# Optimization experiments

Measured on AMD Instinct MI355X. Metric: run time of the kernel, lower is better.

Reference implementation:

```python
import jax, jax.numpy as jnp
import numpy as np

EPS = 1e-8
LAMBDA_SOFTMAX = 20.0
TEMPERATURE = 0.05


def l2norm(x, axis):
    # matches torch: x / (sqrt(sum(x^2)) + eps)
    return x / (jnp.sqrt(jnp.sum(x * x, axis=axis, keepdims=True)) + EPS)


def func_attention_fast(query, context, query_mask, context_mask):
    """query (Bq,Lq,d), context (Bc,Ls,d), query_mask (Bq,Lq,1), context_mask (Bc,1,Ls).
    Returns weightedContext (Bc,Bq,Lq,d)."""
    q = l2norm(query, -1)
    c = l2norm(context, -1)
    # context.unsqueeze(1) @ query^T -> (Bc,Bq,Ls,Lq)
    attn = jnp.einsum('csd,qld->cqsl', c, q)
    attn = jnp.where(attn > 0, attn, 0.1 * attn)  # LeakyReLU(0.1)
    attn = l2norm(attn, 3)                        # normalize over Lq axis
    attn = jnp.transpose(attn, (0, 1, 3, 2))      # (Bc,Bq,Lq,Ls)
    attn = attn + query_mask[None] + context_mask[:, None]
    attn = jax.nn.softmax(attn * LAMBDA_SOFTMAX, axis=-1)
    # focal_type='prob' -> funcH = 1.0
    re_attn = attn / jnp.sum(attn, axis=-1, keepdims=True)
    # contextT @ re_attnT then transpose -> (Bc,Bq,Lq,d)
    return jnp.einsum('csd,cqls->cqld', c, re_attn)


def cosine_sim(x1, x2):
    w12 = jnp.sum(x1 * x2, axis=-1)
    w1 = jnp.linalg.norm(x1, axis=-1)
    w2 = jnp.linalg.norm(x2, axis=-1)
    return w12 / jnp.clip(w1 * w2, 1e-8)


def xattn_score_fast(images, captions, img_mask, cap_mask):
    # i2t: attend image regions for each caption word
    wei = func_attention_fast(captions, images, cap_mask[:, :, None], img_mask[:, None, :])
    i2t_sim = cosine_sim(captions[None], wei).mean(axis=-1)   # (n_img, n_cap)
    # t2i: attend caption words for each image region
    wei = func_attention_fast(images, captions, img_mask[:, :, None], cap_mask[:, None, :])
    t2i_sim = cosine_sim(images[None], wei).mean(axis=-1)     # (n_cap, n_img)
    return t2i_sim.T + i2t_sim                                # (n_img, n_cap)


def norm_softmax_loss(x):
    i_logsm = jax.nn.log_softmax(x / TEMPERATURE, axis=1)
    j_logsm = jax.nn.log_softmax(x.T / TEMPERATURE, axis=1)
    return -jnp.mean(jnp.diag(i_logsm)) - jnp.mean(jnp.diag(j_logsm))


def rwa_loss(im, s, im_m, s_m):
    scores = xattn_score_fast(im, s, im_m, s_m)               # (B,B)
    labels = jnp.eye(im.shape[0], dtype=scores.dtype)
    logits = scores * LAMBDA_SOFTMAX
    pred = jax.nn.softmax(logits, axis=1)
    loss = pred * (jax.nn.log_softmax(logits, axis=1) - jnp.log(labels + 1e-6))
    return jnp.mean(jnp.sum(loss, axis=1))


def setup_inputs() -> dict:
    key = jax.random.key(0)
    k1, k2, k3, k4 = jax.random.split(key, 4)
    B, Lr, Lw, d = 128, 64, 32, 512
    return {
        'global_sim': jax.random.normal(k1, (B, B), dtype=jnp.float32),
        'local_im': jax.random.normal(k2, (B, Lr, d), dtype=jnp.float32),
        'local_s': jax.random.normal(k3, (B, Lw, d), dtype=jnp.float32),
        'local_im_m': jnp.zeros((B, Lr), dtype=jnp.float32),
        'local_s_l': jax.random.randint(k4, (B,), 1, Lw, dtype=jnp.int32),
        'local_s_m': jnp.zeros((B, Lw), dtype=jnp.float32),
    }


def reference(global_sim, local_im, local_s, local_im_m, local_s_l, local_s_m):
    # use_local=True, use_global=True (local_s_l is unused in the fast path)
    global_loss = norm_softmax_loss(global_sim)
    local_loss = rwa_loss(local_im, local_s, local_im_m, local_s_m)
    loss = global_loss + local_loss
    return (loss, global_loss, local_loss)
```

## Files before the change

### kernel.cpp

```cpp
#include <hip/hip_runtime.h>
#include <math.h>

#define EPSF 1e-8f
#define LAM 20.0f

typedef short short8 __attribute__((ext_vector_type(8)));
typedef float f32x4 __attribute__((ext_vector_type(4)));

__device__ __forceinline__ unsigned short f2bf(float x) {
  unsigned u = __float_as_uint(x);
  u += 0x7fffu + ((u >> 16) & 1u);
  return (unsigned short)(u >> 16);
}
__device__ __forceinline__ float bf2f(unsigned short h) {
  return __uint_as_float(((unsigned)h) << 16);
}

__global__ __launch_bounds__(256) void norm_convert(
    const float* __restrict__ im, const float* __restrict__ s,
    float* __restrict__ nim, float* __restrict__ ns,
    unsigned short* __restrict__ imn, unsigned short* __restrict__ sn,
    float* __restrict__ acc) {
  if (blockIdx.x == 0 && threadIdx.x < 4) acc[threadIdx.x] = 0.f;
  int row = blockIdx.x * 4 + (threadIdx.x >> 6);
  int lane = threadIdx.x & 63;
  const float* src;
  unsigned short* dst;
  float* ndst;
  if (row < 8192) {
    src = im + ((size_t)row << 9);
    dst = imn + ((size_t)row << 9);
    ndst = nim + row;
  } else {
    int r = row - 8192;
    src = s + ((size_t)r << 9);
    dst = sn + ((size_t)r << 9);
    ndst = ns + r;
  }
  float4 v0 = ((const float4*)src)[lane * 2];
  float4 v1 = ((const float4*)src)[lane * 2 + 1];
  float ss = 0.f;
  ss = fmaf(v0.x, v0.x, ss); ss = fmaf(v0.y, v0.y, ss);
  ss = fmaf(v0.z, v0.z, ss); ss = fmaf(v0.w, v0.w, ss);
  ss = fmaf(v1.x, v1.x, ss); ss = fmaf(v1.y, v1.y, ss);
  ss = fmaf(v1.z, v1.z, ss); ss = fmaf(v1.w, v1.w, ss);
#pragma unroll
  for (int o = 32; o; o >>= 1) ss += __shfl_xor(ss, o);
  float n = sqrtf(ss);
  if (lane == 0) *ndst = n;
  float ci = 1.0f / (n + EPSF);
  union { unsigned short us[8]; uint4 v; } p;
  p.us[0] = f2bf(v0.x * ci); p.us[1] = f2bf(v0.y * ci);
  p.us[2] = f2bf(v0.z * ci); p.us[3] = f2bf(v0.w * ci);
  p.us[4] = f2bf(v1.x * ci); p.us[5] = f2bf(v1.y * ci);
  p.us[6] = f2bf(v1.z * ci); p.us[7] = f2bf(v1.w * ci);
  ((uint4*)dst)[lane] = p.v;
}

template <int LS>
__device__ __forceinline__ void gram_body(const unsigned short* __restrict__ ctxn,
                                          unsigned short* __restrict__ Gbf,
                                          int c, char* sm) {
  constexpr int RW = (LS / 16) / 2;
  const int t = threadIdx.x;
  const int w = t >> 6, lane = t & 63, m16 = lane & 15, grp = lane >> 4;
  const int rT0 = (w & 1) * RW, cT0 = (w >> 1) * RW;
  const unsigned short* base = ctxn + ((size_t)c * LS << 9);
  f32x4 g[RW][RW];
#pragma unroll
  for (int ri = 0; ri < RW; ri++)
#pragma unroll
    for (int ci = 0; ci < RW; ci++) g[ri][ci] = {0.f, 0.f, 0.f, 0.f};

  for (int ch = 0; ch < 4; ch++) {
    __syncthreads();
    for (int idx = t; idx < LS * 16; idx += 256) {
      int row = idx >> 4, u = idx & 15;
      *(uint4*)(sm + row * 272 + u * 16) =
          ((const uint4*)(base + ((size_t)row << 9) + (ch << 7)))[u];
    }
    __syncthreads();
#pragma unroll
    for (int kk = 0; kk < 4; kk++) {
      short8 a[RW], b[RW];
#pragma unroll
      for (int ri = 0; ri < RW; ri++)
        a[ri] = *(const short8*)(sm + ((rT0 + ri) * 16 + m16) * 272 + kk * 64 + grp * 16);
#pragma unroll
      for (int ci = 0; ci < RW; ci++)
        b[ci] = *(const short8*)(sm + ((cT0 + ci) * 16 + m16) * 272 + kk * 64 + grp * 16);
#pragma unroll
      for (int ri = 0; ri < RW; ri++)
#pragma unroll
        for (int ci = 0; ci < RW; ci++)
          g[ri][ci] = __builtin_amdgcn_mfma_f32_16x16x32_bf16(a[ri], b[ci], g[ri][ci], 0, 0, 0);
    }
  }
#pragma unroll
  for (int ri = 0; ri < RW; ri++)
#pragma unroll
    for (int ci = 0; ci < RW; ci++)
#pragma unroll
      for (int r = 0; r < 4; r++) {
        int s = (rT0 + ri) * 16 + grp * 4 + r;
        int sp = (cT0 + ci) * 16 + m16;
        Gbf[(size_t)c * LS * LS + s * LS + sp] = f2bf(g[ri][ci][r]);
      }
}

__global__ __launch_bounds__(256, 2) void gram_all(
    const unsigned short* __restrict__ imn, const unsigned short* __restrict__ sn,
    unsigned short* __restrict__ Gim, unsigned short* __restrict__ Gs) {
  __shared__ __align__(16) char sm[64 * 272];
  if (blockIdx.x < 128) gram_body<64>(imn, Gim, blockIdx.x, sm);
  else gram_body<32>(sn, Gs, blockIdx.x - 128, sm);
}

__global__ __launch_bounds__(256, 3) void attn_pair(
    const unsigned short* __restrict__ imn, const unsigned short* __restrict__ sn,
    const unsigned short* __restrict__ Gim, const unsigned short* __restrict__ Gs,
    const float* __restrict__ nim, const float* __restrict__ ns,
    const float* __restrict__ im_m, const float* __restrict__ s_m,
    float* __restrict__ i2t, float* __restrict__ t2i) {
  constexpr int SROW = 144;
  constexpr int S0P = 264;
  constexpr int GOFF = 256 * SROW;
  constexpr int FOFF = GOFF + 8192;
  constexpr int POFF = 33792;
  __shared__ __align__(16) char sm[FOFF + 2056 * 4];
  float* F = (float*)(sm + FOFF);
  float* rinv_i = F;
  float* cmv_i = F + 512;
  float* cmmax_i = F + 640;
  float* rinv_t = F + 644;
  float* sevt = F + 900;
  float* wn2t = F + 1412;
  float* cmv_t = F + 1924;
  float* cmmax_t = F + 2052;
  float* sumev_i = F + 644;
  float* psum = (float*)(sm + GOFF);

  const int bq = blockIdx.x;
  const int bc = blockIdx.y;
  const int t = threadIdx.x;
  const int w = t >> 6, lane = t & 63, m16 = lane & 15, grp = lane >> 4;
  auto soff = [](int n) { return n * S0P; };

  const unsigned short* aBase = imn + ((size_t)bc << 16);
  const unsigned short* bBase = sn + ((size_t)bq << 16);

  if (t < 128) cmv_i[t] = im_m[bc * 128 + t];
  else cmv_t[t - 128] = s_m[bq * 128 + (t - 128)];
  const int c3 = w >> 1, hf = w & 1;
  short8 g_a[2][2];
  {
    const unsigned short* gB = Gim + ((size_t)bc * 2 + c3) * 4096;
#pragma unroll
    for (int mi = 0; mi < 2; mi++) {
      int sp = (hf * 2 + mi) * 16 + m16;
#pragma unroll
      for (int ks = 0; ks < 2; ks++)
        g_a[mi][ks] = *(const short8*)(gB + sp * 64 + ks * 32 + grp * 8);
    }
  }

  f32x4 regs[16];
#pragma unroll
  for (int i = 0; i < 16; i++) regs[i] = {0.f, 0.f, 0.f, 0.f};

  const int sT0 = (w & 1) * 4, nT0 = (w >> 1) * 4;
  for (int ch = 0; ch < 8; ch++) {
    __syncthreads();
#pragma unroll
    for (int i = 0; i < 8; i++) {
      int idx = t + i * 256;
      int row = idx >> 3, u = idx & 7;
      const unsigned short* src =
          (row < 128) ? (aBase + ((size_t)row << 9)) : (bBase + ((size_t)(row - 128) << 9));
      *(uint4*)(sm + row * SROW + u * 16) = *(const uint4*)(src + ch * 64 + u * 8);
    }
    __syncthreads();
#pragma unroll
    for (int kk = 0; kk < 2; kk++) {
      short8 av[4], bv[4];
#pragma unroll
      for (int si = 0; si < 4; si++)
        av[si] = *(const short8*)(sm + ((sT0 + si) * 16 + m16) * SROW + kk * 64 + grp * 16);
#pragma unroll
      for (int ni = 0; ni < 4; ni++)
        bv[ni] = *(const short8*)(sm + (128 + (nT0 + ni) * 16 + m16) * SROW + kk * 64 + grp * 16);
#pragma unroll
      for (int si = 0; si < 4; si++)
#pragma unroll
        for (int ni = 0; ni < 4; ni++)
          regs[si * 4 + ni] = __builtin_amdgcn_mfma_f32_16x16x32_bf16(
              av[si], bv[ni], regs[si * 4 + ni], 0, 0, 0);
    }
  }
  __syncthreads();
#pragma unroll
  for (int si = 0; si < 4; si++)
#pragma unroll
    for (int ni = 0; ni < 4; ni++) {
      int n = (nT0 + ni) * 16 + m16;
      int m0 = (sT0 + si) * 16 + grp * 4;
      f32x4 a = regs[si * 4 + ni];
      ushort4 p;
      p.x = f2bf(a[0]); p.y = f2bf(a[1]);
      p.z = f2bf(a[2]); p.w = f2bf(a[3]);
      *(ushort4*)(sm + soff(n) + m0 * 2) = p;
    }
  __syncthreads();

  if (t < 128) {
    if (t < 2) {
      float mx = cmv_i[t * 64];
      for (int s = 1; s < 64; s++) mx = fmaxf(mx, cmv_i[t * 64 + s]);
      cmmax_i[t] = mx;
    } else if (t < 6) {
      int ci = t - 2;
      float mx = cmv_t[ci * 32];
      for (int s = 1; s < 32; s++) mx = fmaxf(mx, cmv_t[ci * 32 + s]);
      cmmax_t[ci] = mx;
    }
    int qi = t >> 5, mg = (t & 31) * 4;
    float s0 = 0.f, s1 = 0.f, s2 = 0.f, s3 = 0.f;
    for (int l = 0; l < 32; l++) {
      uint2 pk = *(const uint2*)(sm + soff(qi * 32 + l) + mg * 2);
      float v0 = __uint_as_float(pk.x << 16);
      float v1 = __uint_as_float(pk.x & 0xffff0000u);
      float v2 = __uint_as_float(pk.y << 16);
      float v3 = __uint_as_float(pk.y & 0xffff0000u);
      v0 = v0 > 0.f ? v0 : 0.1f * v0;
      v1 = v1 > 0.f ? v1 : 0.1f * v1;
      v2 = v2 > 0.f ? v2 : 0.1f * v2;
      v3 = v3 > 0.f ? v3 : 0.1f * v3;
      s0 = fmaf(v0, v0, s0); s1 = fmaf(v1, v1, s1);
      s2 = fmaf(v2, v2, s2); s3 = fmaf(v3, v3, s3);
    }
    rinv_i[qi * 128 + mg + 0] = 1.0f / (sqrtf(s0) + EPSF);
    rinv_i[qi * 128 + mg + 1] = 1.0f / (sqrtf(s1) + EPSF);
    rinv_i[qi * 128 + mg + 2] = 1.0f / (sqrtf(s2) + EPSF);
    rinv_i[qi * 128 + mg + 3] = 1.0f / (sqrtf(s3) + EPSF);
  } else {
    int n = t - 128;
#pragma unroll
    for (int qi = 0; qi < 2; qi++) {
      float ss = 0.f;
#pragma unroll 4
      for (int j = 0; j < 16; j++) {
        uint2 pk = *(const uint2*)(sm + soff(n) + qi * 128 + j * 8);
        float v0 = __uint_as_float(pk.x << 16);
        float v1 = __uint_as_float(pk.x & 0xffff0000u);
        float v2 = __uint_as_float(pk.y << 16);
        float v3 = __uint_as_float(pk.y & 0xffff0000u);
        v0 = v0 > 0.f ? v0 : 0.1f * v0;
        v1 = v1 > 0.f ? v1 : 0.1f * v1;
        v2 = v2 > 0.f ? v2 : 0.1f * v2;
        v3 = v3 > 0.f ? v3 : 0.1f * v3;
        ss = fmaf(v0, v0, ss); ss = fmaf(v1, v1, ss);
        ss = fmaf(v2, v2, ss); ss = fmaf(v3, v3, ss);
      }
      rinv_t[qi * 128 + n] = 1.0f / (sqrtf(ss) + EPSF);
    }
  }
  __syncthreads();

  {
    const int mp = t & 127;
    const int h = t >> 7;
    const int qi = mp >> 6;
    char* ET = sm + GOFF;
    float* P = (float*)(sm + POFF);
    const unsigned short* gB2 = Gs + ((size_t)bq << 12);
    for (int ci = 0; ci < 4; ci++) {
      short8 ga0 = *(const short8*)(gB2 + ci * 1024 + m16 * 32 + grp * 8);
      short8 ga1 = *(const short8*)(gB2 + ci * 1024 + (16 + m16) * 32 + grp * 8);
      const float mxc = LAM * (1.0f + cmmax_t[ci]);
      const float* rv = rinv_t + qi * 128 + ci * 32 + h * 16;
      const float* cv = cmv_t + ci * 32 + h * 16;
      float sev = 0.f;
      unsigned pk[8];
#pragma unroll
      for (int u = 0; u < 8; u++) {
        int s0 = ci * 32 + h * 16 + u * 2;
        float v0 = bf2f(*(const unsigned short*)(sm + soff(s0) + mp * 2));
        float v1 = bf2f(*(const unsigned short*)(sm + soff(s0 + 1) + mp * 2));
        float l0 = v0 > 0.f ? v0 : 0.1f * v0;
        float l1 = v1 > 0.f ? v1 : 0.1f * v1;
        float e0 = __expf(LAM * fmaf(l0, rv[u * 2], cv[u * 2]) - mxc);
        float e1 = __expf(LAM * fmaf(l1, rv[u * 2 + 1], cv[u * 2 + 1]) - mxc);
        sev = fmaf(e0, v0, sev);
        sev = fmaf(e1, v1, sev);
        pk[u] = (unsigned)f2bf(e0) | ((unsigned)f2bf(e1) << 16);
      }
      P[t] = sev;
      uint4 w0; w0.x = pk[0]; w0.y = pk[1]; w0.z = pk[2]; w0.w = pk[3];
      uint4 w1; w1.x = pk[4]; w1.y = pk[5]; w1.z = pk[6]; w1.w = pk[7];
      *(uint4*)(ET + mp * 64 + h * 32) = w0;
      *(uint4*)(ET + mp * 64 + h * 32 + 16) = w1;
      __syncthreads();
      if (t < 128) sevt[ci * 128 + t] = P[t] + P[t + 128];
      short8 bfrag[2];
#pragma unroll
      for (int nt = 0; nt < 2; nt++)
        bfrag[nt] = *(const short8*)(ET + ((w * 2 + nt) * 16 + m16) * 64 + grp * 16);
      f32x4 u00 = __builtin_amdgcn_mfma_f32_16x16x32_bf16(ga0, bfrag[0], (f32x4){0.f, 0.f, 0.f, 0.f}, 0, 0, 0);
      f32x4 u01 = __builtin_amdgcn_mfma_f32_16x16x32_bf16(ga0, bfrag[1], (f32x4){0.f, 0.f, 0.f, 0.f}, 0, 0, 0);
      f32x4 u10 = __builtin_amdgcn_mfma_f32_16x16x32_bf16(ga1, bfrag[0], (f32x4){0.f, 0.f, 0.f, 0.f}, 0, 0, 0);
      f32x4 u11 = __builtin_amdgcn_mfma_f32_16x16x32_bf16(ga1, bfrag[1], (f32x4){0.f, 0.f, 0.f, 0.f}, 0, 0, 0);
#pragma unroll
      for (int nt = 0; nt < 2; nt++) {
        const char* erow = ET + ((w * 2 + nt) * 16 + m16) * 64;
        float part = 0.f;
#pragma unroll
        for (int mt = 0; mt < 2; mt++) {
          uint2 ee = *(const uint2*)(erow + (mt * 16 + grp * 4) * 2);
          f32x4 uu = (mt == 0) ? (nt == 0 ? u00 : u01) : (nt == 0 ? u10 : u11);
          part += __uint_as_float(ee.x << 16) * uu[0];
          part += __uint_as_float(ee.x & 0xffff0000u) * uu[1];
          part += __uint_as_float(ee.y << 16) * uu[2];
          part += __uint_as_float(ee.y & 0xffff0000u) * uu[3];
        }
        part += __shfl_xor(part, 16);
        part += __shfl_xor(part, 32);
        if (lane < 16) wn2t[ci * 128 + (w * 2 + nt) * 16 + m16] = part;
      }
      __syncthreads();
    }
  }

  {
    const int p = t >> 5, l0 = t & 31;
    const int cc = p >> 1, qi = p & 1;
    float sum = 0.f;
#pragma unroll
    for (int li = 0; li < 2; li++) {
      int n = qi * 64 + l0 + li * 32;
      float nq = nim[bc * 128 + n];
      float sev = sevt[cc * 128 + n];
      float wn2 = wn2t[cc * 128 + n];
      float denom = fmaxf(nq * sqrtf(fmaxf(wn2, 0.f)), 1e-30f);
      sum += (nq + EPSF) * sev / denom;
    }
#pragma unroll
    for (int o = 1; o < 32; o <<= 1) sum += __shfl_xor(sum, o);
    if (l0 == 0) t2i[(bq * 4 + cc) * 128 + bc * 2 + qi] = sum * (1.0f / 64.f);
  }
  __syncthreads();

  {
    const int n = t & 127;
    const int qi = n >> 5;
    const int ci = t >> 7;
    char* rowp = sm + soff(n) + ci * 128;
    const float* rv = rinv_i + qi * 128 + ci * 64;
    const float* cv = cmv_i + ci * 64;
    const float mxc = LAM * (1.0f + cmmax_i[ci]);
    float sev = 0.f;
#pragma unroll
    for (int u = 0; u < 16; u++) {
      uint2 pk = *(const uint2*)(rowp + u * 8);
      float v0 = __uint_as_float(pk.x << 16);
      float v1 = __uint_as_float(pk.x & 0xffff0000u);
      float v2 = __uint_as_float(pk.y << 16);
      float v3 = __uint_as_float(pk.y & 0xffff0000u);
      int s = u * 4;
      float l0 = v0 > 0.f ? v0 : 0.1f * v0;
      float l1 = v1 > 0.f ? v1 : 0.1f * v1;
      float l2 = v2 > 0.f ? v2 : 0.1f * v2;
      float l3 = v3 > 0.f ? v3 : 0.1f * v3;
      float e0 = __expf(LAM * fmaf(l0, rv[s + 0], cv[s + 0]) - mxc);
      float e1 = __expf(LAM * fmaf(l1, rv[s + 1], cv[s + 1]) - mxc);
      float e2 = __expf(LAM * fmaf(l2, rv[s + 2], cv[s + 2]) - mxc);
      float e3 = __expf(LAM * fmaf(l3, rv[s + 3], cv[s + 3]) - mxc);
      sev = fmaf(e0, v0, sev); sev = fmaf(e1, v1, sev);
      sev = fmaf(e2, v2, sev); sev = fmaf(e3, v3, sev);
      uint2 o;
      o.x = (unsigned)f2bf(e0) | ((unsigned)f2bf(e1) << 16);
      o.y = (unsigned)f2bf(e2) | ((unsigned)f2bf(e3) << 16);
      *(uint2*)(rowp + u * 8) = o;
    }
    sumev_i[ci * 128 + n] = sev;
  }
  __syncthreads();

  {
#pragma unroll
    for (int i = 0; i < 16; i++) regs[i] = {0.f, 0.f, 0.f, 0.f};
#pragma unroll
    for (int ks = 0; ks < 2; ks++) {
      short8 b2[8];
#pragma unroll
      for (int nt = 0; nt < 8; nt++) {
        const char* p = sm + soff(nt * 16 + m16) + c3 * 128 + ks * 64 + grp * 16;
        union { uint2 h[2]; short8 v; } bb;
        bb.h[0] = *(const uint2*)(p);
        bb.h[1] = *(const uint2*)(p + 8);
        b2[nt] = bb.v;
      }
#pragma unroll
      for (int mi = 0; mi < 2; mi++)
#pragma unroll
        for (int nt = 0; nt < 8; nt++)
          regs[mi * 8 + nt] = __builtin_amdgcn_mfma_f32_16x16x32_bf16(
              g_a[mi][ks], b2[nt], regs[mi * 8 + nt], 0, 0, 0);
    }
    float wp[8];
#pragma unroll
    for (int nt = 0; nt < 8; nt++) wp[nt] = 0.f;
#pragma unroll
    for (int nt = 0; nt < 8; nt++) {
#pragma unroll
      for (int mi = 0; mi < 2; mi++) {
        int sp = (hf * 2 + mi) * 16 + grp * 4;
        uint2 ee = *(const uint2*)(sm + soff(nt * 16 + m16) + (c3 * 64 + sp) * 2);
        f32x4 uu = regs[mi * 8 + nt];
        wp[nt] += __uint_as_float(ee.x << 16) * uu[0] +
                  __uint_as_float(ee.x & 0xffff0000u) * uu[1] +
                  __uint_as_float(ee.y << 16) * uu[2] +
                  __uint_as_float(ee.y & 0xffff0000u) * uu[3];
      }
    }
#pragma unroll
    for (int o = 16; o < 64; o <<= 1)
#pragma unroll
      for (int nt = 0; nt < 8; nt++) wp[nt] += __shfl_xor(wp[nt], o);
    if (lane < 16) {
#pragma unroll
      for (int nt = 0; nt < 8; nt++) psum[w * 128 + nt * 16 + lane] = wp[nt];
    }
  }
  __syncthreads();

  {
    const int p = t >> 5, l0 = t & 31;
    const int cc = p >> 2, qi = p & 3;
    int n = qi * 32 + l0;
    float nq = ns[bq * 128 + n];
    float sev = sumev_i[cc * 128 + n];
    float wn2u = psum[(cc * 2 + 0) * 128 + n] + psum[(cc * 2 + 1) * 128 + n];
    float denom = fmaxf(nq * sqrtf(fmaxf(wn2u, 0.f)), 1e-30f);
    float sum = (nq + EPSF) * sev / denom;
#pragma unroll
    for (int o = 1; o < 32; o <<= 1) sum += __shfl_xor(sum, o);
    if (l0 == 0) i2t[(bc * 2 + cc) * 128 + bq * 4 + qi] = sum * (1.0f / 32.f);
  }
}

__global__ __launch_bounds__(128) void loss_fused(
    const float* __restrict__ gsim, const float* __restrict__ i2t,
    const float* __restrict__ t2i, float* __restrict__ acc,
    float* __restrict__ out) {
  const int i = blockIdx.x, j = threadIdx.x;
  const int B = 128;
  __shared__ float sh[2];
  auto bmax = [&](float v) -> float {
#pragma unroll
    for (int o = 32; o; o >>= 1) v = fmaxf(v, __shfl_down(v, o));
    if ((j & 63) == 0) sh[j >> 6] = v;
    __syncthreads();
    float r = fmaxf(sh[0], sh[1]);
    __syncthreads();
    return r;
  };
  auto bsum = [&](float v) -> float {
#pragma unroll
    for (int o = 32; o; o >>= 1) v += __shfl_down(v, o);
    if ((j & 63) == 0) sh[j >> 6] = v;
    __syncthreads();
    float r = sh[0] + sh[1];
    __syncthreads();
    return r;
  };
  float xr = gsim[i * B + j] * 20.f;
  float xc = gsim[j * B + i] * 20.f;
  float sc = (i2t[i * B + j] + t2i[j * B + i]) * LAM;
  float mr = bmax(xr);
  float lser = mr + logf(bsum(__expf(xr - mr)));
  float mc = bmax(xc);
  float lsec = mc + logf(bsum(__expf(xc - mc)));
  float ml = bmax(sc);
  float lsel = ml + logf(bsum(__expf(sc - ml)));
  float pred = __expf(sc - lsel);
  float logLab = (i == j) ? logf(1.0f + 1e-6f) : logf(1e-6f);
  float tsum = bsum(pred * (sc - lsel - logLab));
  if (j == 0) {
    float d = gsim[i * B + i] * 20.f;
    atomicAdd(&acc[0], d - lser);
    atomicAdd(&acc[1], d - lsec);
    atomicAdd(&acc[2], tsum);
    __threadfence();
    unsigned old = atomicAdd((unsigned*)&acc[3], 1u);
    if (old == 127u) {
      __threadfence();
      float a = acc[0], b = acc[1], c = acc[2];
      float gl = -(a / 128.f) - (b / 128.f);
      float ll = c / 128.f;
      out[0] = gl + ll;
      out[1] = gl;
      out[2] = ll;
    }
  }
}

extern "C" void kernel_launch(void* const* d_in, const int* in_sizes, int n_in,
                              void* d_out, int out_size, void* d_ws,
                              size_t ws_size, hipStream_t stream) {
  const float* gsim = (const float*)d_in[0];
  const float* im = (const float*)d_in[1];
  const float* s = (const float*)d_in[2];
  const float* im_m = (const float*)d_in[3];
  const float* s_m = (const float*)d_in[5];
  float* out = (float*)d_out;

  float* ws = (float*)d_ws;
  float* nim = ws;
  float* ns = ws + 8192;
  float* i2t = ws + 12288;
  float* t2i = ws + 28672;
  float* acc = ws + 45056;
  unsigned short* Gim = (unsigned short*)(ws + 45440);
  unsigned short* Gs = (unsigned short*)(ws + 307584);
  unsigned short* imn = (unsigned short*)(ws + 373120);
  unsigned short* sn = (unsigned short*)(ws + 2470272);

  norm_convert<<<dim3(3072), dim3(256), 0, stream>>>(im, s, nim, ns, imn, sn, acc);
  gram_all<<<dim3(256), dim3(256), 0, stream>>>(imn, sn, Gim, Gs);
  attn_pair<<<dim3(32, 64), dim3(256), 0, stream>>>(imn, sn, Gim, Gs, nim, ns,
                                                    im_m, s_m, i2t, t2i);
  loss_fused<<<dim3(128), dim3(128), 0, stream>>>(gsim, i2t, t2i, acc, out);
}
```

Measured before the change: 184.4 us.

## Stage attention Gram tiles via direct global-to-LDS loads with XOR-swizzled layout

Replaces the register-staged copy of the query/context chunk into padded shared memory with global_load_lds direct transfers into an unpadded 128-byte-row layout. An XOR swizzle on 16-byte columns keeps the MFMA fragment reads free of bank conflicts. The exp-matrix ET tile is also XOR-swizzled on both its writes and reads to reduce LDS bank conflicts. This saves VGPR traffic and padding, but it depends on correct swizzle indexing and on the wave-to-rows mapping of the direct loads.

```diff
diff --git a/kernel.cpp b/kernel.cpp
--- a/kernel.cpp
+++ b/kernel.cpp
@@ -14,6 +14,11 @@
 }
 __device__ __forceinline__ float bf2f(unsigned short h) {
   return __uint_as_float(((unsigned)h) << 16);
+}
+__device__ __forceinline__ void gload_lds16(const void* g, void* l) {
+  __builtin_amdgcn_global_load_lds(
+      (const __attribute__((address_space(1))) void*)g,
+      (__attribute__((address_space(3))) void*)l, 16, 0, 0);
 }
 
 __global__ __launch_bounds__(256) void norm_convert(
@@ -122,9 +127,8 @@
     const float* __restrict__ nim, const float* __restrict__ ns,
     const float* __restrict__ im_m, const float* __restrict__ s_m,
     float* __restrict__ i2t, float* __restrict__ t2i) {
-  constexpr int SROW = 144;
   constexpr int S0P = 264;
-  constexpr int GOFF = 256 * SROW;
+  constexpr int GOFF = 36864;
   constexpr int FOFF = GOFF + 8192;
   constexpr int POFF = 33792;
   __shared__ __align__(16) char sm[FOFF + 2056 * 4];
@@ -169,26 +173,29 @@
   for (int i = 0; i < 16; i++) regs[i] = {0.f, 0.f, 0.f, 0.f};
 
   const int sT0 = (w & 1) * 4, nT0 = (w >> 1) * 4;
+  const int r_lane = lane >> 3, c_lane = lane & 7;
+  const unsigned short* wbase = (w < 2) ? (aBase + ((size_t)(w * 64) << 9))
+                                        : (bBase + ((size_t)((w - 2) * 64) << 9));
+  const unsigned short* pb = wbase + r_lane * 512 + ((c_lane ^ r_lane) << 3);
+  char* ldsw = sm + w * 8192;
+  const int sx = m16 & 7;
   for (int ch = 0; ch < 8; ch++) {
     __syncthreads();
 #pragma unroll
-    for (int i = 0; i < 8; i++) {
-      int idx = t + i * 256;
-      int row = idx >> 3, u = idx & 7;
-      const unsigned short* src =
-          (row < 128) ? (aBase + ((size_t)row << 9)) : (bBase + ((size_t)(row - 128) << 9));
-      *(uint4*)(sm + row * SROW + u * 16) = *(const uint4*)(src + ch * 64 + u * 8);
-    }
+    for (int j = 0; j < 8; j++)
+      gload_lds16(pb + ch * 64 + j * 4096, ldsw + j * 1024);
     __syncthreads();
 #pragma unroll
     for (int kk = 0; kk < 2; kk++) {
       short8 av[4], bv[4];
 #pragma unroll
       for (int si = 0; si < 4; si++)
-        av[si] = *(const short8*)(sm + ((sT0 + si) * 16 + m16) * SROW + kk * 64 + grp * 16);
+        av[si] = *(const short8*)(sm + (((sT0 + si) * 16 + m16) << 7) +
+                                  (((kk * 4 + grp) ^ sx) << 4));
 #pragma unroll
       for (int ni = 0; ni < 4; ni++)
-        bv[ni] = *(const short8*)(sm + (128 + (nT0 + ni) * 16 + m16) * SROW + kk * 64 + grp * 16);
+        bv[ni] = *(const short8*)(sm + ((128 + (nT0 + ni) * 16 + m16) << 7) +
+                                  (((kk * 4 + grp) ^ sx) << 4));
 #pragma unroll
       for (int si = 0; si < 4; si++)
 #pragma unroll
@@ -273,6 +280,8 @@
     char* ET = sm + GOFF;
     float* P = (float*)(sm + POFF);
     const unsigned short* gB2 = Gs + ((size_t)bq << 12);
+    const int esw = (mp >> 1) & 3;
+    const int rsw = (m16 >> 1) & 3;
     for (int ci = 0; ci < 4; ci++) {
       short8 ga0 = *(const short8*)(gB2 + ci * 1024 + m16 * 32 + grp * 8);
       short8 ga1 = *(const short8*)(gB2 + ci * 1024 + (16 + m16) * 32 + grp * 8);
@@ -297,25 +306,28 @@
       P[t] = sev;
       uint4 w0; w0.x = pk[0]; w0.y = pk[1]; w0.z = pk[2]; w0.w = pk[3];
       uint4 w1; w1.x = pk[4]; w1.y = pk[5]; w1.z = pk[6]; w1.w = pk[7];
-      *(uint4*)(ET + mp * 64 + h * 32) = w0;
-      *(uint4*)(ET + mp * 64 + h * 32 + 16) = w1;
+      char* rowp = ET + mp * 64;
+      *(uint4*)(rowp + (((2 * h) ^ esw) << 4)) = w0;
+      *(uint4*)(rowp + (((2 * h + 1) ^ esw) << 4)) = w1;
       __syncthreads();
       if (t < 128) sevt[ci * 128 + t] = P[t] + P[t + 128];
       short8 bfrag[2];
 #pragma unroll
       for (int nt = 0; nt < 2; nt++)
-        bfrag[nt] = *(const short8*)(ET + ((w * 2 + nt) * 16 + m16) * 64 + grp * 16);
+        bfrag[nt] = *(const short8*)(ET + (((w * 2 + nt) * 16 + m16) << 6) +
+                                     ((grp ^ rsw) << 4));
       f32x4 u00 = __builtin_amdgcn_mfma_f32_16x16x32_bf16(ga0, bfrag[0], (f32x4){0.f, 0.f, 0.f, 0.f}, 0, 0, 0);
       f32x4 u01 = __builtin_amdgcn_mfma_f32_16x16x32_bf16(ga0, bfrag[1], (f32x4){0.f, 0.f, 0.f, 0.f}, 0, 0, 0);
       f32x4 u10 = __builtin_amdgcn_mfma_f32_16x16x32_bf16(ga1, bfrag[0], (f32x4){0.f, 0.f, 0.f, 0.f}, 0, 0, 0);
       f32x4 u11 = __builtin_amdgcn_mfma_f32_16x16x32_bf16(ga1, bfrag[1], (f32x4){0.f, 0.f, 0.f, 0.f}, 0, 0, 0);
 #pragma unroll
       for (int nt = 0; nt < 2; nt++) {
-        const char* erow = ET + ((w * 2 + nt) * 16 + m16) * 64;
+        const char* erow = ET + (((w * 2 + nt) * 16 + m16) << 6);
         float part = 0.f;
 #pragma unroll
         for (int mt = 0; mt < 2; mt++) {
-          uint2 ee = *(const uint2*)(erow + (mt * 16 + grp * 4) * 2);
+          int cch = 2 * mt + (grp >> 1);
+          uint2 ee = *(const uint2*)(erow + ((cch ^ rsw) << 4) + ((grp & 1) << 3));
           f32x4 uu = (mt == 0) ? (nt == 0 ? u00 : u01) : (nt == 0 ? u10 : u11);
           part += __uint_as_float(ee.x << 16) * uu[0];
           part += __uint_as_float(ee.x & 0xffff0000u) * uu[1];
```

Result: faster. 177.3 us (-3.8%).
